# Kernel optimization log

Measured on AMD Instinct MI355X. Metric: run time of the kernel, lower is better.

## Reference

```python
import jax, jax.numpy as jnp
import numpy as np

K = 3  # kernel_size=(3,3), flat all-ones structuring element


def _erode(x):
    # flat erosion = sliding-window min, SAME padding with +inf (geodesic)
    return jax.lax.reduce_window(x, float('inf'), jax.lax.min,
                                 (1, 1, K, K), (1, 1, 1, 1), 'SAME')


def _dilate(x):
    # flat dilation = sliding-window max, SAME padding with -inf
    return jax.lax.reduce_window(x, -float('inf'), jax.lax.max,
                                 (1, 1, K, K), (1, 1, 1, 1), 'SAME')


def setup_inputs() -> dict:
    key = jax.random.key(0)
    x = jax.random.uniform(key, (16, 3, 1024, 1024), dtype=jnp.float32)
    return {"x": x}


def reference(x) -> jnp.ndarray:
    # morphological opening: dilation(erosion(x)) with flat 3x3 SE,
    # applied per-channel (kernel repeated over channels in the original)
    return _dilate(_erode(x))
```

## Files before the change

kernel.cpp:

```cpp
#include <hip/hip_runtime.h>


#define W 1024
#define H 1024
#define ROWS 32
#define NT 256

__global__ __launch_bounds__(NT)
void open3x3_reg(const float* __restrict__ in, float* __restrict__ out) {
    const int t  = threadIdx.x;
    const int c0 = 4 * t;
    const int y0 = blockIdx.y * ROWS;
    const size_t imgoff = (size_t)blockIdx.z * (size_t)(W * H);
    const float* img  = in  + imgoff;
    float*       outp = out + imgoff;

    const float PINF = __builtin_inff();
    const float NINF = -__builtin_inff();

    const bool has_l = (t > 0);
    const bool has_r = (t < NT-1);

    auto load_row = [&](int r, float x[8]) {
        if (r >= 0 && r < H) {
            const float* p = img + r * W;
            float4 m = *(const float4*)(p + c0);
            x[2] = m.x; x[3] = m.y; x[4] = m.z; x[5] = m.w;
            x[0] = has_l ? p[c0 - 2] : PINF;
            x[1] = has_l ? p[c0 - 1] : PINF;
            x[6] = has_r ? p[c0 + 4] : PINF;
            x[7] = has_r ? p[c0 + 5] : PINF;
        } else {
            #pragma unroll
            for (int i = 0; i < 8; i++) x[i] = PINF;
        }
    };
    auto hmin6 = [&](const float x[8], float hm[6]) {
        #pragma unroll
        for (int i = 0; i < 6; i++) hm[i] = fminf(fminf(x[i], x[i+1]), x[i+2]);
    };
    auto erow = [&](int r, const float a[6], const float b[6], const float c[6],
                    float e[6]) {
        if (r >= 0 && r < H) {
            #pragma unroll
            for (int i = 0; i < 6; i++) e[i] = fminf(fminf(a[i], b[i]), c[i]);
            if (!has_l) e[0] = NINF;
            if (!has_r) e[5] = NINF;
        } else {
            #pragma unroll
            for (int i = 0; i < 6; i++) e[i] = NINF;
        }
    };
    auto hmax4 = [&](const float e[6], float hx[4]) {
        #pragma unroll
        for (int i = 0; i < 4; i++) hx[i] = fmaxf(fmaxf(e[i], e[i+1]), e[i+2]);
    };

    float x[8];
    float hmP[6], hmQ[6], hmR[6], e[6];
    float hx0[4], hx1[4], hx2[4];

    load_row(y0 - 2, x); hmin6(x, hmP);
    load_row(y0 - 1, x); hmin6(x, hmQ);
    load_row(y0,     x); hmin6(x, hmR);
    erow(y0 - 1, hmP, hmQ, hmR, e); hmax4(e, hx0);

    #pragma unroll
    for (int i = 0; i < 6; i++) { hmP[i] = hmQ[i]; hmQ[i] = hmR[i]; }
    load_row(y0 + 1, x); hmin6(x, hmR);
    erow(y0, hmP, hmQ, hmR, e); hmax4(e, hx1);
    #pragma unroll
    for (int i = 0; i < 6; i++) { hmP[i] = hmQ[i]; hmQ[i] = hmR[i]; }

    float xc[8];
    load_row(y0 + 2, xc);

    #pragma unroll 4
    for (int k = 0; k < ROWS; k++) {
        const int y = y0 + k;
        float xn[8];
        if (k + 1 < ROWS) load_row(y + 3, xn);

        hmin6(xc, hmR);
        erow(y + 1, hmP, hmQ, hmR, e);
        hmax4(e, hx2);

        float4 o;
        o.x = fmaxf(fmaxf(hx0[0], hx1[0]), hx2[0]);
        o.y = fmaxf(fmaxf(hx0[1], hx1[1]), hx2[1]);
        o.z = fmaxf(fmaxf(hx0[2], hx1[2]), hx2[2]);
        o.w = fmaxf(fmaxf(hx0[3], hx1[3]), hx2[3]);
        *(float4*)(outp + (size_t)y * W + c0) = o;

        #pragma unroll
        for (int i = 0; i < 4; i++) { hx0[i] = hx1[i]; hx1[i] = hx2[i]; }
        #pragma unroll
        for (int i = 0; i < 6; i++) { hmP[i] = hmQ[i]; hmQ[i] = hmR[i]; }
        #pragma unroll
        for (int i = 0; i < 8; i++) xc[i] = xn[i];
    }
}

extern "C" void kernel_launch(void* const* d_in, const int* in_sizes, int n_in,
                              void* d_out, int out_size, void* d_ws, size_t ws_size,
                              hipStream_t stream) {
    const float* x = (const float*)d_in[0];
    float* out = (float*)d_out;
    dim3 grid(1, H / ROWS, 48);
    dim3 block(NT);
    open3x3_reg<<<grid, block, 0, stream>>>(x, out);
}
```

Before: 353.3 us.

## Share halo columns via wavefront shuffles and deepen row prefetch pipeline

Replaces the per-thread scalar halo loads with cross-lane shuffles, so only wave-edge lanes issue extra loads for neighbour columns. Prefetches three rows ahead through a rotating register buffer and fully unrolls the row loop to hide global-load latency. Halves rows per block to double the block count and switches output to nontemporal stores to avoid polluting the cache. In exchange the halo overhead per block rises, since four extra rows are read for every sixteen produced, and register pressure goes up from the deeper prefetch.

```diff
diff --git a/kernel.cpp b/kernel.cpp
--- a/kernel.cpp
+++ b/kernel.cpp
@@ -3,44 +3,67 @@
 
 #define W 1024
 #define H 1024
-#define ROWS 32
+#define ROWS 16
 #define NT 256
 
+typedef float nvec4 __attribute__((ext_vector_type(4)));
+
+struct Row { float4 m; float eA, eB; };
+
 __global__ __launch_bounds__(NT)
-void open3x3_reg(const float* __restrict__ in, float* __restrict__ out) {
-    const int t  = threadIdx.x;
-    const int c0 = 4 * t;
-    const int y0 = blockIdx.y * ROWS;
-    const size_t imgoff = (size_t)blockIdx.z * (size_t)(W * H);
+void open3x3_v3(const float* __restrict__ in, float* __restrict__ out) {
+    const int t    = threadIdx.x;
+    const int lane = t & 63;
+    const int c0   = 4 * t;
+    const int y0   = blockIdx.x * ROWS;
+    const size_t imgoff = (size_t)blockIdx.y * (size_t)(W * H);
     const float* img  = in  + imgoff;
     float*       outp = out + imgoff;
 
     const float PINF = __builtin_inff();
     const float NINF = -__builtin_inff();
+    const bool is_l  = (lane == 0);
+    const bool is_r  = (lane == 63);
+    const bool has_l = (c0 > 0);
+    const bool has_r = (c0 + 4 < W);
 
-    const bool has_l = (t > 0);
-    const bool has_r = (t < NT-1);
-
-    auto load_row = [&](int r, float x[8]) {
+    auto load_row = [&](int r) -> Row {
+        Row R;
         if (r >= 0 && r < H) {
             const float* p = img + r * W;
-            float4 m = *(const float4*)(p + c0);
-            x[2] = m.x; x[3] = m.y; x[4] = m.z; x[5] = m.w;
-            x[0] = has_l ? p[c0 - 2] : PINF;
-            x[1] = has_l ? p[c0 - 1] : PINF;
-            x[6] = has_r ? p[c0 + 4] : PINF;
-            x[7] = has_r ? p[c0 + 5] : PINF;
+            R.m = *(const float4*)(p + c0);
+            float a = PINF, b = PINF;
+            if ((is_l && has_l) || (is_r && has_r)) {
+                int ec = is_l ? (c0 - 2) : (c0 + 4);
+                a = p[ec]; b = p[ec + 1];
+            }
+            R.eA = a; R.eB = b;
         } else {
-            #pragma unroll
-            for (int i = 0; i < 8; i++) x[i] = PINF;
+            R.m = make_float4(PINF, PINF, PINF, PINF);
+            R.eA = PINF; R.eB = PINF;
         }
+        return R;
     };
-    auto hmin6 = [&](const float x[8], float hm[6]) {
-        #pragma unroll
-        for (int i = 0; i < 6; i++) hm[i] = fminf(fminf(x[i], x[i+1]), x[i+2]);
+
+    auto hmin6 = [&](const Row& R, float hm[6]) {
+        float x0 = __shfl_up(R.m.z, 1);
+        float x1 = __shfl_up(R.m.w, 1);
+        float x6 = __shfl_down(R.m.x, 1);
+        float x7 = __shfl_down(R.m.y, 1);
+        x0 = is_l ? R.eA : x0;
+        x1 = is_l ? R.eB : x1;
+        x6 = is_r ? R.eA : x6;
+        x7 = is_r ? R.eB : x7;
+        const float x2 = R.m.x, x3 = R.m.y, x4 = R.m.z, x5 = R.m.w;
+        hm[0] = fminf(fminf(x0, x1), x2);
+        hm[1] = fminf(fminf(x1, x2), x3);
+        hm[2] = fminf(fminf(x2, x3), x4);
+        hm[3] = fminf(fminf(x3, x4), x5);
+        hm[4] = fminf(fminf(x4, x5), x6);
+        hm[5] = fminf(fminf(x5, x6), x7);
     };
-    auto erow = [&](int r, const float a[6], const float b[6], const float c[6],
-                    float e[6]) {
+
+    auto erow = [&](int r, const float a[6], const float b[6], const float c[6], float e[6]) {
         if (r >= 0 && r < H) {
             #pragma unroll
             for (int i = 0; i < 6; i++) e[i] = fminf(fminf(a[i], b[i]), c[i]);
@@ -51,53 +74,51 @@
             for (int i = 0; i < 6; i++) e[i] = NINF;
         }
     };
+
     auto hmax4 = [&](const float e[6], float hx[4]) {
         #pragma unroll
-        for (int i = 0; i < 4; i++) hx[i] = fmaxf(fmaxf(e[i], e[i+1]), e[i+2]);
+        for (int i = 0; i < 4; i++) hx[i] = fmaxf(fmaxf(e[i], e[i + 1]), e[i + 2]);
     };
 
-    float x[8];
-    float hmP[6], hmQ[6], hmR[6], e[6];
-    float hx0[4], hx1[4], hx2[4];
+    Row r0 = load_row(y0 - 2);
+    Row r1 = load_row(y0 - 1);
+    Row r2 = load_row(y0);
+    Row r3 = load_row(y0 + 1);
+    Row buf[3];
+    buf[0] = load_row(y0 + 2);
+    buf[1] = load_row(y0 + 3);
+    buf[2] = load_row(y0 + 4);
 
-    load_row(y0 - 2, x); hmin6(x, hmP);
-    load_row(y0 - 1, x); hmin6(x, hmQ);
-    load_row(y0,     x); hmin6(x, hmR);
-    erow(y0 - 1, hmP, hmQ, hmR, e); hmax4(e, hx0);
+    float hmA[6], hmB[6], hmC[6], hmD[6];
+    hmin6(r0, hmA); hmin6(r1, hmB); hmin6(r2, hmC); hmin6(r3, hmD);
+    float e[6], hx0[4], hx1[4], hx2[4];
+    erow(y0 - 1, hmA, hmB, hmC, e); hmax4(e, hx0);
+    erow(y0,     hmB, hmC, hmD, e); hmax4(e, hx1);
+    float hmP[6], hmQ[6], hmR[6];
+    #pragma unroll
+    for (int i = 0; i < 6; i++) { hmP[i] = hmC[i]; hmQ[i] = hmD[i]; }
 
     #pragma unroll
-    for (int i = 0; i < 6; i++) { hmP[i] = hmQ[i]; hmQ[i] = hmR[i]; }
-    load_row(y0 + 1, x); hmin6(x, hmR);
-    erow(y0, hmP, hmQ, hmR, e); hmax4(e, hx1);
-    #pragma unroll
-    for (int i = 0; i < 6; i++) { hmP[i] = hmQ[i]; hmQ[i] = hmR[i]; }
-
-    float xc[8];
-    load_row(y0 + 2, xc);
-
-    #pragma unroll 4
     for (int k = 0; k < ROWS; k++) {
         const int y = y0 + k;
-        float xn[8];
-        if (k + 1 < ROWS) load_row(y + 3, xn);
+        Row cur = buf[k % 3];
+        if (k < ROWS - 3) buf[k % 3] = load_row(y + 5);
 
-        hmin6(xc, hmR);
+        hmin6(cur, hmR);
         erow(y + 1, hmP, hmQ, hmR, e);
         hmax4(e, hx2);
 
-        float4 o;
+        nvec4 o;
         o.x = fmaxf(fmaxf(hx0[0], hx1[0]), hx2[0]);
         o.y = fmaxf(fmaxf(hx0[1], hx1[1]), hx2[1]);
         o.z = fmaxf(fmaxf(hx0[2], hx1[2]), hx2[2]);
         o.w = fmaxf(fmaxf(hx0[3], hx1[3]), hx2[3]);
-        *(float4*)(outp + (size_t)y * W + c0) = o;
+        __builtin_nontemporal_store(o, (nvec4*)(outp + (size_t)y * W + c0));
 
         #pragma unroll
         for (int i = 0; i < 4; i++) { hx0[i] = hx1[i]; hx1[i] = hx2[i]; }
         #pragma unroll
         for (int i = 0; i < 6; i++) { hmP[i] = hmQ[i]; hmQ[i] = hmR[i]; }
-        #pragma unroll
-        for (int i = 0; i < 8; i++) xc[i] = xn[i];
     }
 }
 
@@ -106,7 +127,7 @@
                               hipStream_t stream) {
     const float* x = (const float*)d_in[0];
     float* out = (float*)d_out;
-    dim3 grid(1, H / ROWS, 48);
+    dim3 grid(H / ROWS, 48);
     dim3 block(NT);
-    open3x3_reg<<<grid, block, 0, stream>>>(x, out);
+    open3x3_v3<<<grid, block, 0, stream>>>(x, out);
 }
```

After: 343.4 us. 1.03x faster.
